# Kernel tuning notes

Hardware: AMD Instinct MI355X
Metric: run time of the kernel (lower is better)

Reference implementation:

```python
import jax, jax.numpy as jnp
import numpy as np

WIN = 9  # window_size from init


def _box_filter_3d(x, k):
    """Separable normalized box filter over the 3 spatial dims of NCDHW x.
    Mathematically identical to a dense k^3 mean filter with SAME padding."""
    c = x.shape[1]
    pad = k // 2
    for axis in range(3):
        kshape = [1, 1, 1]
        kshape[axis] = k
        kern = jnp.ones((c, 1, *kshape), x.dtype) / k  # depthwise, normalized per-axis
        padding = [(pad, pad) if a == axis else (0, 0) for a in range(3)]
        x = jax.lax.conv_general_dilated(
            x, kern, window_strides=(1, 1, 1), padding=padding,
            dimension_numbers=('NCDHW', 'OIDHW', 'NCDHW'),
            feature_group_count=c)
    return x


def setup_inputs() -> dict:
    key = jax.random.key(0)
    k1, k2 = jax.random.split(key)
    shape = (1, 1, 192, 192, 192)
    pred = jax.random.uniform(k1, shape, dtype=jnp.float32)
    target = jax.random.uniform(k2, shape, dtype=jnp.float32)
    return {"pred": pred, "target": target}


def reference(pred, target):
    Ii, Ji = target, pred
    # local means of I, J, I^2, J^2, IJ via one grouped (5-channel) box filter
    all_five = jnp.concatenate([Ii, Ji, Ii * Ii, Ji * Ji, Ii * Ji], axis=1)
    f = _box_filter_3d(all_five, WIN)
    mu1, mu2 = f[:, 0:1], f[:, 1:2]
    conv_I2, conv_J2, conv_IJ = f[:, 2:3], f[:, 3:4], f[:, 4:5]
    sigma1_sq = conv_I2 - mu1 * mu1
    sigma2_sq = conv_J2 - mu2 * mu2
    sigma12 = conv_IJ - mu1 * mu2
    eps = jnp.finfo(sigma12.dtype).eps
    cc = sigma12 * sigma12 / (sigma1_sq * sigma2_sq + eps)
    return 1.0 - jnp.mean(cc)
```

## Files before the change

kernel.cpp:

```cpp
#include <hip/hip_runtime.h>
#include <hip/hip_bf16.h>

#define SDIM 192
#define S2 (SDIM*SDIM)
#define S3 ((size_t)SDIM*S2)
#define NCH 5
#define RAD 4

#define STRH 8
#define RROW 16
#define RQU 224
#define WSTR 96
#define NSTRIP (SDIM/STRH)
#define SQQ(Q) ((Q) + ((Q) >> 3))

#define KB_THR 128
#define KB_KBC 4
#define KB_POSB (S2/(KB_THR*KB_KBC))
#define KB_DCH 12
#define KB_NDC (SDIM/KB_DCH)
#define KB_GRID (KB_POSB*KB_NDC)
#define NPART KB_GRID

__device__ __forceinline__ unsigned packbf(float lo, float hi) {
    __hip_bfloat162 h2 = __float22bfloat162_rn(make_float2(lo, hi));
    unsigned u; __builtin_memcpy(&u, &h2, 4); return u;
}
__device__ __forceinline__ float ulo(unsigned u) { return __uint_as_float(u << 16); }
__device__ __forceinline__ float uhi(unsigned u) { return __uint_as_float(u & 0xffff0000u); }

__global__ __launch_bounds__(256) void ka_wh(const float* __restrict__ pred,
                                             const float* __restrict__ tgt,
                                             unsigned* __restrict__ BU) {
    const int b = blockIdx.x;
    const int strip = b % NSTRIP;
    const int d = b / NSTRIP;
    const int h0 = strip * STRH;
    const size_t dbase = (size_t)d * S2;
    const int t = threadIdx.x;

    __shared__ unsigned IJ[RROW][RQU];
    __shared__ unsigned wfU[NCH][RROW][WSTR];

    if (t < RROW * 8) {
        const int r = t >> 3, p = t & 7;
        const int col = (p < 4) ? p : (216 + p);
        IJ[r][col] = 0u;
    }
    const float4* tg4 = (const float4*)tgt;
    const float4* pr4 = (const float4*)pred;
#pragma unroll
    for (int it = 0; it < 3; ++it) {
        const int u = t + 256 * it;
        const int r = u / 48, q = u % 48;
        const int hh = h0 - RAD + r;
        float4 vi = make_float4(0.f, 0.f, 0.f, 0.f), vj = vi;
        if (hh >= 0 && hh < SDIM) {
            const size_t gi = (dbase + (size_t)hh * SDIM) / 4 + q;
            vi = tg4[gi]; vj = pr4[gi];
        }
        uint4 w;
        w.x = packbf(vi.x, vj.x); w.y = packbf(vi.y, vj.y);
        w.z = packbf(vi.z, vj.z); w.w = packbf(vi.w, vj.w);
        *(uint4*)&IJ[r][4 * SQQ(q + 1)] = w;
    }
    __syncthreads();

#pragma unroll
    for (int it = 0; it < 3; ++it) {
        const int u = t + 256 * it;
        const int row = u / 48, cu = u % 48;
        const uint4 a  = *(const uint4*)&IJ[row][4 * SQQ(cu)];
        const uint4 bq = *(const uint4*)&IJ[row][4 * SQQ(cu + 1)];
        const uint4 cq = *(const uint4*)&IJ[row][4 * SQQ(cu + 2)];
        unsigned raw[12] = {a.x, a.y, a.z, a.w, bq.x, bq.y, bq.z, bq.w,
                            cq.x, cq.y, cq.z, cq.w};
        float fi[12], fj[12];
#pragma unroll
        for (int k = 0; k < 12; ++k) { fi[k] = ulo(raw[k]); fj[k] = uhi(raw[k]); }

#define W4(CH, EXPR) { \
        float pv[12]; \
        _Pragma("unroll") for (int k = 0; k < 12; ++k) pv[k] = (EXPR); \
        float s0 = 0.f; \
        _Pragma("unroll") for (int k = 0; k < 9; ++k) s0 += pv[k]; \
        const float s1 = s0 - pv[0] + pv[9]; \
        const float s2 = s1 - pv[1] + pv[10]; \
        const float s3 = s2 - pv[2] + pv[11]; \
        uint2 o; o.x = packbf(s0, s1); o.y = packbf(s2, s3); \
        *(uint2*)&wfU[CH][row][2 * cu] = o; }

        W4(0, fi[k])
        W4(1, fj[k])
        W4(2, fi[k] * fi[k])
        W4(3, fj[k] * fj[k])
        W4(4, fi[k] * fj[k])
#undef W4
    }
    __syncthreads();

#pragma unroll
    for (int it = 0; it < 2; ++it) {
        const int col = t + 256 * it;
        if (col < NCH * 96) {
            const int c = col / 96, wp = col % 96;
            float lo[RROW], hi[RROW];
#pragma unroll
            for (int r = 0; r < RROW; ++r) {
                const unsigned v = wfU[c][r][wp];
                lo[r] = ulo(v); hi[r] = uhi(v);
            }
            float slo = 0.f, shi = 0.f;
#pragma unroll
            for (int r = 0; r < 9; ++r) { slo += lo[r]; shi += hi[r]; }
            unsigned* dst = BU + (size_t)c * (S3 / 2) + (dbase + (size_t)h0 * SDIM) / 2 + wp;
            dst[0] = packbf(slo, shi);
#pragma unroll
            for (int hr = 1; hr < STRH; ++hr) {
                slo += lo[hr + 8] - lo[hr - 1];
                shi += hi[hr + 8] - hi[hr - 1];
                dst[hr * (SDIM / 2)] = packbf(slo, shi);
            }
        }
    }
}

#define SLICE2(s, OP) { const size_t sb = ((size_t)(s) * S2 + pos0) >> 2; \
    _Pragma("unroll") for (int c = 0; c < NCH; ++c) { \
        const uint2 v = B2[(size_t)c * (S3 >> 2) + sb]; \
        z[c][0] OP ulo(v.x); z[c][1] OP uhi(v.x); \
        z[c][2] OP ulo(v.y); z[c][3] OP uhi(v.y); } }

__global__ __launch_bounds__(KB_THR) void kb_d_cc(const unsigned* __restrict__ BU,
                                                  float* __restrict__ partials) {
    const int bid = blockIdx.x;
    const int dc = bid / KB_POSB;
    const int pb = bid % KB_POSB;
    const int d0 = dc * KB_DCH;
    const int pos0 = pb * (KB_THR * KB_KBC) + threadIdx.x * KB_KBC;
    const uint2* B2 = (const uint2*)BU;

    float z[NCH][KB_KBC];
#pragma unroll
    for (int c = 0; c < NCH; ++c)
#pragma unroll
        for (int i = 0; i < KB_KBC; ++i) z[c][i] = 0.f;

#pragma unroll
    for (int dd = -RAD; dd <= RAD; ++dd) {
        const int s = d0 + dd;
        if (s >= 0 && s < SDIM) SLICE2(s, +=)
    }

    const float inv = 1.0f / 729.0f;
    const float eps = 1.1920929e-07f;
    float acc = 0.f;

#pragma unroll
    for (int k = 0; k < KB_DCH; ++k) {
        const int d = d0 + k;
#pragma unroll
        for (int i = 0; i < KB_KBC; ++i) {
            const float mu1 = z[0][i] * inv;
            const float mu2 = z[1][i] * inv;
            const float sg1 = z[2][i] * inv - mu1 * mu1;
            const float sg2 = z[3][i] * inv - mu2 * mu2;
            const float s12 = z[4][i] * inv - mu1 * mu2;
            acc += (s12 * s12) * __builtin_amdgcn_rcpf(sg1 * sg2 + eps);
        }
        const int da = d + RAD + 1;
        const int ds = d - RAD;
        if (da < SDIM) SLICE2(da, +=)
        if (ds >= 0)   SLICE2(ds, -=)
    }

    __shared__ float red[KB_THR];
    red[threadIdx.x] = acc;
    __syncthreads();
#pragma unroll
    for (int o = KB_THR / 2; o > 0; o >>= 1) {
        if (threadIdx.x < o) red[threadIdx.x] += red[threadIdx.x + o];
        __syncthreads();
    }
    if (threadIdx.x == 0) partials[bid] = red[0];
}

__global__ __launch_bounds__(256) void k4_finalize(const float* __restrict__ partials,
                                                   float* __restrict__ out) {
    __shared__ float sm[256];
    float s = 0.f;
    for (int i = threadIdx.x; i < NPART; i += 256) s += partials[i];
    sm[threadIdx.x] = s;
    __syncthreads();
#pragma unroll
    for (int o = 128; o > 0; o >>= 1) {
        if (threadIdx.x < o) sm[threadIdx.x] += sm[threadIdx.x + o];
        __syncthreads();
    }
    if (threadIdx.x == 0) out[0] = 1.0f - sm[0] / (float)((size_t)SDIM * S2);
}

extern "C" void kernel_launch(void* const* d_in, const int* in_sizes, int n_in,
                              void* d_out, int out_size, void* d_ws, size_t ws_size,
                              hipStream_t stream) {
    const float* pred = (const float*)d_in[0];
    const float* tgt  = (const float*)d_in[1];
    float* out = (float*)d_out;

    const size_t b_bytes = (size_t)NCH * S3 * sizeof(__hip_bfloat16);
    const size_t b_pad = (b_bytes + 255) & ~(size_t)255;

    unsigned* BU = (unsigned*)d_ws;
    float* partials = (float*)((char*)d_ws + b_pad);

    ka_wh<<<SDIM * NSTRIP, 256, 0, stream>>>(pred, tgt, BU);
    kb_d_cc<<<KB_GRID, KB_THR, 0, stream>>>(BU, partials);
    k4_finalize<<<1, 256, 0, stream>>>(partials, out);
}
```

Baseline: 76.85 us.

## Fuse W/H box pass and D-sliding CC into one tiled kernel

```diff
diff --git a/kernel.cpp b/kernel.cpp
--- a/kernel.cpp
+++ b/kernel.cpp
@@ -3,24 +3,26 @@
 
 #define SDIM 192
 #define S2 (SDIM*SDIM)
-#define S3 ((size_t)SDIM*S2)
 #define NCH 5
 #define RAD 4
 
-#define STRH 8
-#define RROW 16
-#define RQU 224
-#define WSTR 96
-#define NSTRIP (SDIM/STRH)
-#define SQQ(Q) ((Q) + ((Q) >> 3))
+#define TW 64
+#define TH 8
+#define NWT (SDIM/TW)
+#define NHT (SDIM/TH)
+#define DCH 12
+#define NDC (SDIM/DCH)
+#define NSTEP (DCH + 2*RAD)
+#define FGRID (NWT*NHT*NDC)
+#define NPART FGRID
 
-#define KB_THR 128
-#define KB_KBC 4
-#define KB_POSB (S2/(KB_THR*KB_KBC))
-#define KB_DCH 12
-#define KB_NDC (SDIM/KB_DCH)
-#define KB_GRID (KB_POSB*KB_NDC)
-#define NPART KB_GRID
+#define SROW 16
+#define SQN 20
+#define SQS(Q) ((Q) + ((Q) >> 3))
+#define IJW 88
+#define WFP 33
+
+typedef float v2f __attribute__((ext_vector_type(2)));
 
 __device__ __forceinline__ unsigned packbf(float lo, float hi) {
     __hip_bfloat162 h2 = __float22bfloat162_rn(make_float2(lo, hi));
@@ -29,160 +31,134 @@
 __device__ __forceinline__ float ulo(unsigned u) { return __uint_as_float(u << 16); }
 __device__ __forceinline__ float uhi(unsigned u) { return __uint_as_float(u & 0xffff0000u); }
 
-__global__ __launch_bounds__(256) void ka_wh(const float* __restrict__ pred,
-                                             const float* __restrict__ tgt,
-                                             unsigned* __restrict__ BU) {
+__global__ __launch_bounds__(256) void fused_ncc(const float* __restrict__ pred,
+                                                 const float* __restrict__ tgt,
+                                                 float* __restrict__ partials) {
     const int b = blockIdx.x;
-    const int strip = b % NSTRIP;
-    const int d = b / NSTRIP;
-    const int h0 = strip * STRH;
-    const size_t dbase = (size_t)d * S2;
+    const int wt = b % NWT;
+    const int ht = (b / NWT) % NHT;
+    const int dc = b / (NWT * NHT);
+    const int w0 = wt * TW, h0 = ht * TH, d0 = dc * DCH;
     const int t = threadIdx.x;
 
-    __shared__ unsigned IJ[RROW][RQU];
-    __shared__ unsigned wfU[NCH][RROW][WSTR];
+    __shared__ unsigned IJ[SROW][IJW];
+    __shared__ unsigned wfU[NCH][SROW][WFP];
+    __shared__ float red[256];
 
-    if (t < RROW * 8) {
-        const int r = t >> 3, p = t & 7;
-        const int col = (p < 4) ? p : (216 + p);
-        IJ[r][col] = 0u;
-    }
     const float4* tg4 = (const float4*)tgt;
     const float4* pr4 = (const float4*)pred;
+
+    const int wrow = t >> 4, wqu = t & 15;
+    const int hr = t >> 5, wp = t & 31;
+
+    unsigned ring[NCH][9];
+    v2f z[NCH];
 #pragma unroll
-    for (int it = 0; it < 3; ++it) {
-        const int u = t + 256 * it;
-        const int r = u / 48, q = u % 48;
-        const int hh = h0 - RAD + r;
-        float4 vi = make_float4(0.f, 0.f, 0.f, 0.f), vj = vi;
-        if (hh >= 0 && hh < SDIM) {
-            const size_t gi = (dbase + (size_t)hh * SDIM) / 4 + q;
-            vi = tg4[gi]; vj = pr4[gi];
-        }
-        uint4 w;
-        w.x = packbf(vi.x, vj.x); w.y = packbf(vi.y, vj.y);
-        w.z = packbf(vi.z, vj.z); w.w = packbf(vi.w, vj.w);
-        *(uint4*)&IJ[r][4 * SQQ(q + 1)] = w;
+    for (int c = 0; c < NCH; ++c) {
+        z[c] = (v2f)(0.f);
+#pragma unroll
+        for (int k = 0; k < 9; ++k) ring[c][k] = 0u;
     }
-    __syncthreads();
 
+    v2f acc = (v2f)(0.f);
+    const float inv = 1.0f / 729.0f;
+    const float eps = 1.1920929e-07f;
+    const int gq0 = w0 / 4 - 2;
+
+    for (int g = 0; g < 3; ++g) {
 #pragma unroll
-    for (int it = 0; it < 3; ++it) {
-        const int u = t + 256 * it;
-        const int row = u / 48, cu = u % 48;
-        const uint4 a  = *(const uint4*)&IJ[row][4 * SQQ(cu)];
-        const uint4 bq = *(const uint4*)&IJ[row][4 * SQQ(cu + 1)];
-        const uint4 cq = *(const uint4*)&IJ[row][4 * SQQ(cu + 2)];
-        unsigned raw[12] = {a.x, a.y, a.z, a.w, bq.x, bq.y, bq.z, bq.w,
-                            cq.x, cq.y, cq.z, cq.w};
-        float fi[12], fj[12];
+        for (int k9 = 0; k9 < 9; ++k9) {
+            const int k = g * 9 + k9;
+            if (k < NSTEP) {
+                const int sa = d0 - RAD + k;
+                const bool sval = (sa >= 0) && (sa < SDIM);
+                if (sval) {
+                    const size_t sb4 = ((size_t)sa * S2) >> 2;
 #pragma unroll
-        for (int k = 0; k < 12; ++k) { fi[k] = ulo(raw[k]); fj[k] = uhi(raw[k]); }
-
+                    for (int it = 0; it < 2; ++it) {
+                        const int u = t + 256 * it;
+                        if (u < SROW * SQN) {
+                            const int r = u / SQN, sq = u % SQN;
+                            const int hh = h0 - RAD + r;
+                            const int gq = gq0 + sq;
+                            float4 vi = make_float4(0.f,0.f,0.f,0.f), vj = vi;
+                            if (hh >= 0 && hh < SDIM && gq >= 0 && gq < 48) {
+                                const size_t gi = sb4 + (size_t)hh * (SDIM/4) + gq;
+                                vi = tg4[gi]; vj = pr4[gi];
+                            }
+                            uint4 w;
+                            w.x = packbf(vi.x, vj.x); w.y = packbf(vi.y, vj.y);
+                            w.z = packbf(vi.z, vj.z); w.w = packbf(vi.w, vj.w);
+                            *(uint4*)&IJ[r][4 * SQS(sq)] = w;
+                        }
+                    }
+                }
+                __syncthreads();
+                if (sval) {
+                    const uint4 a  = *(const uint4*)&IJ[wrow][4 * SQS(wqu + 1)];
+                    const uint4 bq = *(const uint4*)&IJ[wrow][4 * SQS(wqu + 2)];
+                    const uint4 cq = *(const uint4*)&IJ[wrow][4 * SQS(wqu + 3)];
+                    unsigned raw[12] = {a.x, a.y, a.z, a.w, bq.x, bq.y, bq.z, bq.w,
+                                        cq.x, cq.y, cq.z, cq.w};
+                    float fi[12], fj[12];
+#pragma unroll
+                    for (int kk = 0; kk < 12; ++kk) { fi[kk] = ulo(raw[kk]); fj[kk] = uhi(raw[kk]); }
 #define W4(CH, EXPR) { \
-        float pv[12]; \
-        _Pragma("unroll") for (int k = 0; k < 12; ++k) pv[k] = (EXPR); \
-        float s0 = 0.f; \
-        _Pragma("unroll") for (int k = 0; k < 9; ++k) s0 += pv[k]; \
-        const float s1 = s0 - pv[0] + pv[9]; \
-        const float s2 = s1 - pv[1] + pv[10]; \
-        const float s3 = s2 - pv[2] + pv[11]; \
-        uint2 o; o.x = packbf(s0, s1); o.y = packbf(s2, s3); \
-        *(uint2*)&wfU[CH][row][2 * cu] = o; }
-
-        W4(0, fi[k])
-        W4(1, fj[k])
-        W4(2, fi[k] * fi[k])
-        W4(3, fj[k] * fj[k])
-        W4(4, fi[k] * fj[k])
+                    float pv[12]; \
+                    _Pragma("unroll") for (int kk = 0; kk < 12; ++kk) pv[kk] = (EXPR); \
+                    float s0 = 0.f; \
+                    _Pragma("unroll") for (int kk = 0; kk < 9; ++kk) s0 += pv[kk]; \
+                    const float s1 = s0 - pv[0] + pv[9]; \
+                    const float s2 = s1 - pv[1] + pv[10]; \
+                    const float s3 = s2 - pv[2] + pv[11]; \
+                    uint2 o; o.x = packbf(s0, s1); o.y = packbf(s2, s3); \
+                    *(uint2*)&wfU[CH][wrow][2 * wqu] = o; }
+                    W4(0, fi[kk])
+                    W4(1, fj[kk])
+                    W4(2, fi[kk] * fi[kk])
+                    W4(3, fj[kk] * fj[kk])
+                    W4(4, fi[kk] * fj[kk])
 #undef W4
-    }
-    __syncthreads();
-
+                }
+                __syncthreads();
 #pragma unroll
-    for (int it = 0; it < 2; ++it) {
-        const int col = t + 256 * it;
-        if (col < NCH * 96) {
-            const int c = col / 96, wp = col % 96;
-            float lo[RROW], hi[RROW];
+                for (int c = 0; c < NCH; ++c) {
+                    v2f wv = (v2f)(0.f);
+                    if (sval) {
 #pragma unroll
-            for (int r = 0; r < RROW; ++r) {
-                const unsigned v = wfU[c][r][wp];
-                lo[r] = ulo(v); hi[r] = uhi(v);
-            }
-            float slo = 0.f, shi = 0.f;
-#pragma unroll
-            for (int r = 0; r < 9; ++r) { slo += lo[r]; shi += hi[r]; }
-            unsigned* dst = BU + (size_t)c * (S3 / 2) + (dbase + (size_t)h0 * SDIM) / 2 + wp;
-            dst[0] = packbf(slo, shi);
-#pragma unroll
-            for (int hr = 1; hr < STRH; ++hr) {
-                slo += lo[hr + 8] - lo[hr - 1];
-                shi += hi[hr + 8] - hi[hr - 1];
-                dst[hr * (SDIM / 2)] = packbf(slo, shi);
+                        for (int dh = 0; dh < 9; ++dh) {
+                            const unsigned u = wfU[c][hr + dh][wp];
+                            wv += (v2f){ulo(u), uhi(u)};
+                        }
+                    }
+                    const unsigned pu = sval ? packbf(wv.x, wv.y) : 0u;
+                    const unsigned old = ring[c][k9];
+                    ring[c][k9] = pu;
+                    z[c] += (v2f){ulo(pu), uhi(pu)} - (v2f){ulo(old), uhi(old)};
+                }
+                if (k >= 2 * RAD) {
+                    const v2f mu1 = z[0] * inv, mu2 = z[1] * inv;
+                    const v2f sg1 = z[2] * inv - mu1 * mu1;
+                    const v2f sg2 = z[3] * inv - mu2 * mu2;
+                    const v2f s12 = z[4] * inv - mu1 * mu2;
+                    const v2f den = sg1 * sg2 + eps;
+                    v2f rc;
+                    rc.x = __builtin_amdgcn_rcpf(den.x);
+                    rc.y = __builtin_amdgcn_rcpf(den.y);
+                    acc += s12 * s12 * rc;
+                }
             }
         }
     }
-}
 
-#define SLICE2(s, OP) { const size_t sb = ((size_t)(s) * S2 + pos0) >> 2; \
-    _Pragma("unroll") for (int c = 0; c < NCH; ++c) { \
-        const uint2 v = B2[(size_t)c * (S3 >> 2) + sb]; \
-        z[c][0] OP ulo(v.x); z[c][1] OP uhi(v.x); \
-        z[c][2] OP ulo(v.y); z[c][3] OP uhi(v.y); } }
-
-__global__ __launch_bounds__(KB_THR) void kb_d_cc(const unsigned* __restrict__ BU,
-                                                  float* __restrict__ partials) {
-    const int bid = blockIdx.x;
-    const int dc = bid / KB_POSB;
-    const int pb = bid % KB_POSB;
-    const int d0 = dc * KB_DCH;
-    const int pos0 = pb * (KB_THR * KB_KBC) + threadIdx.x * KB_KBC;
-    const uint2* B2 = (const uint2*)BU;
-
-    float z[NCH][KB_KBC];
-#pragma unroll
-    for (int c = 0; c < NCH; ++c)
-#pragma unroll
-        for (int i = 0; i < KB_KBC; ++i) z[c][i] = 0.f;
-
-#pragma unroll
-    for (int dd = -RAD; dd <= RAD; ++dd) {
-        const int s = d0 + dd;
-        if (s >= 0 && s < SDIM) SLICE2(s, +=)
-    }
-
-    const float inv = 1.0f / 729.0f;
-    const float eps = 1.1920929e-07f;
-    float acc = 0.f;
-
-#pragma unroll
-    for (int k = 0; k < KB_DCH; ++k) {
-        const int d = d0 + k;
-#pragma unroll
-        for (int i = 0; i < KB_KBC; ++i) {
-            const float mu1 = z[0][i] * inv;
-            const float mu2 = z[1][i] * inv;
-            const float sg1 = z[2][i] * inv - mu1 * mu1;
-            const float sg2 = z[3][i] * inv - mu2 * mu2;
-            const float s12 = z[4][i] * inv - mu1 * mu2;
-            acc += (s12 * s12) * __builtin_amdgcn_rcpf(sg1 * sg2 + eps);
-        }
-        const int da = d + RAD + 1;
-        const int ds = d - RAD;
-        if (da < SDIM) SLICE2(da, +=)
-        if (ds >= 0)   SLICE2(ds, -=)
-    }
-
-    __shared__ float red[KB_THR];
-    red[threadIdx.x] = acc;
+    red[t] = acc.x + acc.y;
     __syncthreads();
 #pragma unroll
-    for (int o = KB_THR / 2; o > 0; o >>= 1) {
-        if (threadIdx.x < o) red[threadIdx.x] += red[threadIdx.x + o];
+    for (int o = 128; o > 0; o >>= 1) {
+        if (t < o) red[t] += red[t + o];
         __syncthreads();
     }
-    if (threadIdx.x == 0) partials[bid] = red[0];
+    if (t == 0) partials[b] = red[0];
 }
 
 __global__ __launch_bounds__(256) void k4_finalize(const float* __restrict__ partials,
@@ -207,13 +183,8 @@
     const float* tgt  = (const float*)d_in[1];
     float* out = (float*)d_out;
 
-    const size_t b_bytes = (size_t)NCH * S3 * sizeof(__hip_bfloat16);
-    const size_t b_pad = (b_bytes + 255) & ~(size_t)255;
+    float* partials = (float*)d_ws;
 
-    unsigned* BU = (unsigned*)d_ws;
-    float* partials = (float*)((char*)d_ws + b_pad);
-
-    ka_wh<<<SDIM * NSTRIP, 256, 0, stream>>>(pred, tgt, BU);
-    kb_d_cc<<<KB_GRID, KB_THR, 0, stream>>>(BU, partials);
+    fused_ncc<<<FGRID, 256, 0, stream>>>(pred, tgt, partials);
     k4_finalize<<<1, 256, 0, stream>>>(partials, out);
 }
```

Result: slower. 94.98 us (+23.6%).
